# Kernel tuning notes

Hardware: AMD Instinct MI355X
Metric: run time of the kernel (lower is better)

Reference implementation:

```python
import jax, jax.numpy as jnp
import numpy as np

H, D, E, FOCAL, HID = 8, 32, 16, 4, 256  # heads, att_size, edge types, focal heads, hidden
SCALE = D ** -0.5
B, N = 16, 512


def setup_inputs() -> dict:
    key = jax.random.key(0)
    ks = jax.random.split(key, 16)
    f = lambda i, shape, s=1.0: jax.random.normal(ks[i], shape, jnp.float32) * s
    return {
        "q": f(0, (B, N, HID)),
        "k": f(1, (B, N, HID)),
        "v": f(2, (B, N, HID)),
        "query_edge_emb": f(3, (E, H * D), 0.1),
        "key_edge_emb": f(4, (E, H * D), 0.1),
        "edge_attr": jax.random.randint(ks[5], (B, N, N), 0, E),
        "mask": jax.random.randint(ks[6], (B, N), 0, 2).astype(bool),
        "focal_mask": jax.random.randint(ks[7], (B, N, N), 0, 2).astype(bool),
        "Wq": f(8, (H * D, HID), 0.05), "bq": jnp.zeros((H * D,), jnp.float32),
        "Wk": f(9, (H * D, HID), 0.05), "bk": jnp.zeros((H * D,), jnp.float32),
        "Wv": f(10, (H * D, HID), 0.05), "bv": jnp.zeros((H * D,), jnp.float32),
        "Wo": f(11, (HID, H * D), 0.05), "bo": jnp.zeros((HID,), jnp.float32),
    }


def reference(q, k, v, query_edge_emb, key_edge_emb, edge_attr, mask, focal_mask,
              Wq, bq, Wk, bk, Wv, bv, Wo, bo):
    b, n, _ = q.shape
    # projections -> [B, H, N, D]
    qh = (q @ Wq.T + bq).reshape(b, n, H, D).transpose(0, 2, 1, 3)
    kh = (k @ Wk.T + bk).reshape(b, n, H, D).transpose(0, 2, 1, 3)
    vh = (v @ Wv.T + bv).reshape(b, n, H, D).transpose(0, 2, 1, 3)

    # edge-type embeddings -> [H, E, D]
    qe_emb = query_edge_emb.reshape(E, H, D).transpose(1, 0, 2)
    ke_emb = key_edge_emb.reshape(E, H, D).transpose(1, 0, 2)

    # per-node score against each edge type: [B, H, N, E]
    qe = jnp.einsum('bhnd,hed->bhne', qh, qe_emb)
    ke = jnp.einsum('bhnd,hed->bhne', kh, ke_emb)

    # gather per edge type id: [B, H, N, N]
    idx = jnp.broadcast_to(edge_attr[:, None, :, :], (b, H, n, n))
    edge_bias = jnp.take_along_axis(qe, idx, axis=3) + jnp.take_along_axis(ke, idx, axis=3)

    attn = (jnp.einsum('bhid,bhjd->bhij', qh, kh) + edge_bias) * SCALE

    gh = H - FOCAL
    m_g = jnp.broadcast_to(mask[:, None, None, :], (b, gh, n, n))
    m_f = jnp.broadcast_to(focal_mask[:, None, :, :], (b, FOCAL, n, n))
    m = jnp.concatenate([m_g, m_f], axis=1)
    attn = jnp.where(m, attn, -jnp.inf)
    attn = jax.nn.softmax(attn, axis=3)

    out = jnp.einsum('bhij,bhjd->bhid', attn, vh)
    out = out.transpose(0, 2, 1, 3).reshape(b, n, H * D)
    return out @ Wo.T + bo
```

## Files before the change

### kernel.cpp

```cpp
#include <hip/hip_runtime.h>
#include <math.h>

namespace {

constexpr int B = 16, N = 512, H = 8, D = 32, E = 16, HID = 256;
constexpr float SCALE = 0.17677669529663687f;

typedef __attribute__((ext_vector_type(8))) short short8;
typedef __attribute__((ext_vector_type(4))) float float4v;

__device__ inline short f2bf(float x) {
  union { float f; unsigned u; } v; v.f = x;
  unsigned r = v.u + 0x7fffu + ((v.u >> 16) & 1u);
  return (short)(r >> 16);
}
__device__ inline float bf2f(unsigned short u) {
  union { unsigned u; float f; } v; v.u = ((unsigned)u) << 16; return v.f;
}

__global__ __launch_bounds__(256) void gemm_qkv(
    const float* __restrict__ Xq, const float* __restrict__ Xk, const float* __restrict__ Xv,
    const float* __restrict__ Wq, const float* __restrict__ Wk, const float* __restrict__ Wv,
    const float* __restrict__ bq, const float* __restrict__ bk, const float* __restrict__ bv,
    unsigned short* __restrict__ Ybase)
{
  __shared__ __align__(16) unsigned short As[64][72];
  __shared__ __align__(16) unsigned short Bs[64][72];
  const int z = blockIdx.z;
  const float* X = (z == 0) ? Xq : (z == 1) ? Xk : Xv;
  const float* W = (z == 0) ? Wq : (z == 1) ? Wk : Wv;
  const float* bias = (z == 0) ? bq : (z == 1) ? bk : bv;
  unsigned short* Yh = Ybase + (size_t)z * ((size_t)B * H * N * D);

  const int m0 = blockIdx.x * 64, n0 = blockIdx.y * 64;
  const int t = threadIdx.x, lane = t & 63, w = t >> 6;
  const int quad = lane >> 4, col = lane & 15;
  const int wm = (w & 1) * 32, wn = (w >> 1) * 32;
  const int srow = t >> 2, skk = (t & 3) * 16;
  float4v acc[2][2] = {{{0,0,0,0},{0,0,0,0}},{{0,0,0,0},{0,0,0,0}}};

  for (int kit = 0; kit < 4; ++kit) {
    const int k0 = kit * 64;
    {
      const float* xp = X + (size_t)(m0 + srow) * HID + k0 + skk;
      const float* wp = W + (size_t)(n0 + srow) * HID + k0 + skk;
      float4 x1 = *(const float4*)xp, x2 = *(const float4*)(xp + 4);
      float4 x3 = *(const float4*)(xp + 8), x4 = *(const float4*)(xp + 12);
      float4 w1 = *(const float4*)wp, w2 = *(const float4*)(wp + 4);
      float4 w3 = *(const float4*)(wp + 8), w4 = *(const float4*)(wp + 12);
      short8 xa, xb, wa, wb;
      xa[0]=f2bf(x1.x); xa[1]=f2bf(x1.y); xa[2]=f2bf(x1.z); xa[3]=f2bf(x1.w);
      xa[4]=f2bf(x2.x); xa[5]=f2bf(x2.y); xa[6]=f2bf(x2.z); xa[7]=f2bf(x2.w);
      xb[0]=f2bf(x3.x); xb[1]=f2bf(x3.y); xb[2]=f2bf(x3.z); xb[3]=f2bf(x3.w);
      xb[4]=f2bf(x4.x); xb[5]=f2bf(x4.y); xb[6]=f2bf(x4.z); xb[7]=f2bf(x4.w);
      wa[0]=f2bf(w1.x); wa[1]=f2bf(w1.y); wa[2]=f2bf(w1.z); wa[3]=f2bf(w1.w);
      wa[4]=f2bf(w2.x); wa[5]=f2bf(w2.y); wa[6]=f2bf(w2.z); wa[7]=f2bf(w2.w);
      wb[0]=f2bf(w3.x); wb[1]=f2bf(w3.y); wb[2]=f2bf(w3.z); wb[3]=f2bf(w3.w);
      wb[4]=f2bf(w4.x); wb[5]=f2bf(w4.y); wb[6]=f2bf(w4.z); wb[7]=f2bf(w4.w);
      *(short8*)&As[srow][skk] = xa; *(short8*)&As[srow][skk + 8] = xb;
      *(short8*)&Bs[srow][skk] = wa; *(short8*)&Bs[srow][skk + 8] = wb;
    }
    __syncthreads();
#pragma unroll
    for (int ks = 0; ks < 2; ++ks) {
      const int kk = ks * 32 + quad * 8;
      short8 a0 = *(const short8*)&As[wm + col][kk];
      short8 a1 = *(const short8*)&As[wm + 16 + col][kk];
      short8 b0 = *(const short8*)&Bs[wn + col][kk];
      short8 b1 = *(const short8*)&Bs[wn + 16 + col][kk];
      acc[0][0] = __builtin_amdgcn_mfma_f32_16x16x32_bf16(a0, b0, acc[0][0], 0, 0, 0);
      acc[0][1] = __builtin_amdgcn_mfma_f32_16x16x32_bf16(a0, b1, acc[0][1], 0, 0, 0);
      acc[1][0] = __builtin_amdgcn_mfma_f32_16x16x32_bf16(a1, b0, acc[1][0], 0, 0, 0);
      acc[1][1] = __builtin_amdgcn_mfma_f32_16x16x32_bf16(a1, b1, acc[1][1], 0, 0, 0);
    }
    __syncthreads();
  }
#pragma unroll
  for (int mt = 0; mt < 2; ++mt)
#pragma unroll
    for (int nt = 0; nt < 2; ++nt)
#pragma unroll
      for (int r = 0; r < 4; ++r) {
        const int m = m0 + wm + mt * 16 + quad * 4 + r;
        const int n = n0 + wn + nt * 16 + col;
        const float val = acc[mt][nt][r] + bias[n];
        const int b_ = m >> 9, ii = m & 511, h_ = n >> 5, d_ = n & 31;
        Yh[((size_t)(b_ * H + h_) * N + ii) * D + d_] = (unsigned short)f2bf(val);
      }
}

__global__ __launch_bounds__(256) void gemm_out(
    const unsigned short* __restrict__ X, const float* __restrict__ W,
    const float* __restrict__ bias, float* __restrict__ Yf)
{
  __shared__ __align__(16) unsigned short As[64][72];
  __shared__ __align__(16) unsigned short Bs[64][72];
  const int m0 = blockIdx.x * 64, n0 = blockIdx.y * 64;
  const int t = threadIdx.x, lane = t & 63, w = t >> 6;
  const int quad = lane >> 4, col = lane & 15;
  const int wm = (w & 1) * 32, wn = (w >> 1) * 32;
  const int srow = t >> 2, skk = (t & 3) * 16;
  float4v acc[2][2] = {{{0,0,0,0},{0,0,0,0}},{{0,0,0,0},{0,0,0,0}}};

  for (int kit = 0; kit < 4; ++kit) {
    const int k0 = kit * 64;
    {
      const unsigned short* xp = X + (size_t)(m0 + srow) * HID + k0 + skk;
      *(short8*)&As[srow][skk] = *(const short8*)xp;
      *(short8*)&As[srow][skk + 8] = *(const short8*)(xp + 8);
      const float* wp = W + (size_t)(n0 + srow) * HID + k0 + skk;
      float4 w1 = *(const float4*)wp, w2 = *(const float4*)(wp + 4);
      float4 w3 = *(const float4*)(wp + 8), w4 = *(const float4*)(wp + 12);
      short8 wa, wb;
      wa[0]=f2bf(w1.x); wa[1]=f2bf(w1.y); wa[2]=f2bf(w1.z); wa[3]=f2bf(w1.w);
      wa[4]=f2bf(w2.x); wa[5]=f2bf(w2.y); wa[6]=f2bf(w2.z); wa[7]=f2bf(w2.w);
      wb[0]=f2bf(w3.x); wb[1]=f2bf(w3.y); wb[2]=f2bf(w3.z); wb[3]=f2bf(w3.w);
      wb[4]=f2bf(w4.x); wb[5]=f2bf(w4.y); wb[6]=f2bf(w4.z); wb[7]=f2bf(w4.w);
      *(short8*)&Bs[srow][skk] = wa; *(short8*)&Bs[srow][skk + 8] = wb;
    }
    __syncthreads();
#pragma unroll
    for (int ks = 0; ks < 2; ++ks) {
      const int kk = ks * 32 + quad * 8;
      short8 a0 = *(const short8*)&As[wm + col][kk];
      short8 a1 = *(const short8*)&As[wm + 16 + col][kk];
      short8 b0 = *(const short8*)&Bs[wn + col][kk];
      short8 b1 = *(const short8*)&Bs[wn + 16 + col][kk];
      acc[0][0] = __builtin_amdgcn_mfma_f32_16x16x32_bf16(a0, b0, acc[0][0], 0, 0, 0);
      acc[0][1] = __builtin_amdgcn_mfma_f32_16x16x32_bf16(a0, b1, acc[0][1], 0, 0, 0);
      acc[1][0] = __builtin_amdgcn_mfma_f32_16x16x32_bf16(a1, b0, acc[1][0], 0, 0, 0);
      acc[1][1] = __builtin_amdgcn_mfma_f32_16x16x32_bf16(a1, b1, acc[1][1], 0, 0, 0);
    }
    __syncthreads();
  }
#pragma unroll
  for (int mt = 0; mt < 2; ++mt)
#pragma unroll
    for (int nt = 0; nt < 2; ++nt)
#pragma unroll
      for (int r = 0; r < 4; ++r) {
        const int m = m0 + wm + mt * 16 + quad * 4 + r;
        const int n = n0 + wn + nt * 16 + col;
        Yf[(size_t)m * HID + n] = acc[mt][nt][r] + bias[n];
      }
}

__global__ __launch_bounds__(256) void vtrans(
    const unsigned short* __restrict__ vh, unsigned short* __restrict__ vt)
{
  __shared__ unsigned short tile[32][522];
  const int t = threadIdx.x;
  const size_t base = (size_t)blockIdx.x * N * D;
  for (int idx = t; idx < N * D; idx += 256)
    tile[idx & 31][idx >> 5] = vh[base + idx];
  __syncthreads();
  for (int idx = t; idx < N * D; idx += 256)
    vt[base + idx] = tile[idx >> 9][idx & 511];
}

__global__ __launch_bounds__(256) void qke_kernel(
    const unsigned short* __restrict__ qh, const unsigned short* __restrict__ kh,
    const float* __restrict__ qemb, const float* __restrict__ kemb,
    float* __restrict__ qke)
{
  __shared__ float qs[512], ks[512];
  const int t = threadIdx.x;
  const int r0 = blockIdx.x * 16;
  const size_t base = (size_t)r0 * 32;
  for (int idx = t; idx < 512; idx += 256) {
    qs[idx] = bf2f(qh[base + idx]);
    ks[idx] = bf2f(kh[base + idx]);
  }
  __syncthreads();
  const int r = t >> 4, e = t & 15;
  const int h = ((r0 + r) >> 9) & 7;
  const float* qe = qemb + e * (H * D) + h * D;
  const float* ke = kemb + e * (H * D) + h * D;
  float a = 0.f;
#pragma unroll
  for (int d = 0; d < 32; ++d)
    a += qs[r * 32 + d] * qe[d] + ks[r * 32 + d] * ke[d];
  qke[(size_t)r0 * 16 + t] = a;
}

__global__ __launch_bounds__(256) void detect_bool(
    const unsigned int* __restrict__ buf, int* __restrict__ flag)
{
  __shared__ unsigned wr[4];
  const int t = threadIdx.x, w = t >> 6, lane = t & 63;
  unsigned v = 0;
  for (int idx = t; idx < 4096; idx += 256) v |= buf[idx];
  v |= __shfl_xor(v, 1);  v |= __shfl_xor(v, 2);  v |= __shfl_xor(v, 4);
  v |= __shfl_xor(v, 8);  v |= __shfl_xor(v, 16); v |= __shfl_xor(v, 32);
  if (lane == 0) wr[w] = v;
  __syncthreads();
  if (t == 0) flag[0] = ((wr[0] | wr[1] | wr[2] | wr[3]) > 1u) ? 1 : 0;
}

__global__ __launch_bounds__(256) void pack_kernel(
    const int* __restrict__ ea, const void* __restrict__ maskp,
    const void* __restrict__ fmaskp, const int* __restrict__ flag,
    unsigned char* __restrict__ packed)
{
  __shared__ unsigned char tl[16 * 520];
  const int it = blockIdx.x, b = blockIdx.y, t = threadIdx.x;
  const int i0 = it * 16;
  const int bf = *flag;
  const int* fm32 = (const int*)fmaskp;
  const unsigned char* fm8 = (const unsigned char*)fmaskp;
  const int* mk32 = (const int*)maskp;
  const unsigned char* mk8 = (const unsigned char*)maskp;

  for (int idx = t; idx < 16 * 512; idx += 256) {
    const int m = idx >> 9, j = idx & 511;
    const size_t goff = ((size_t)(b * N) + i0 + m) * N + j;
    const int e = ea[goff] & 15;
    const int fv = bf ? (int)fm8[goff] : fm32[goff];
    const int mv = bf ? (int)mk8[b * N + j] : mk32[b * N + j];
    tl[m * 520 + j] = (unsigned char)(e | (fv ? 16 : 0) | (mv ? 32 : 0));
  }
  __syncthreads();
#pragma unroll
  for (int rep = 0; rep < 2; ++rep) {
    const int j = t * 2 + rep;
    unsigned wd[4];
#pragma unroll
    for (int g = 0; g < 4; ++g) {
      const unsigned b0 = tl[(g * 4 + 0) * 520 + j];
      const unsigned b1 = tl[(g * 4 + 1) * 520 + j];
      const unsigned b2 = tl[(g * 4 + 2) * 520 + j];
      const unsigned b3 = tl[(g * 4 + 3) * 520 + j];
      wd[g] = b0 | (b1 << 8) | (b2 << 16) | (b3 << 24);
    }
    *(uint4*)(packed + ((size_t)(b * 32 + it) * 512 + j) * 16) =
        make_uint4(wd[0], wd[1], wd[2], wd[3]);
  }
}

__global__ __launch_bounds__(256, 3) void attn_mfma(
    const unsigned short* __restrict__ qh, const unsigned short* __restrict__ kh,
    const unsigned short* __restrict__ vt, const float* __restrict__ qke,
    const unsigned char* __restrict__ packed, unsigned short* __restrict__ ctx)
{
  __shared__ __align__(16) unsigned char tileT[512 * 16];
  __shared__ __align__(16) unsigned short P[4][16][136];
  __shared__ float qesS[2][16][17];
  __shared__ float ored[4][2][16][33];
  __shared__ float2 wlm[4][2][16];
  __shared__ float scl[4][32];
  __shared__ float linv[32];

  const int it = blockIdx.x, p = blockIdx.y, b = blockIdx.z;
  const int i0 = it * 16;
  const int t = threadIdx.x, w = t >> 6, lane = t & 63;
  const int quad = lane >> 4, col = lane & 15;

  {
    const unsigned char* pt = packed + ((size_t)(b * 32 + it) * 512) * 16;
    const int j0s = w * 128 + lane;
    *(uint4*)&tileT[(size_t)j0s * 16] = *(const uint4*)(pt + (size_t)j0s * 16);
    *(uint4*)&tileT[(size_t)(j0s + 64) * 16] =
        *(const uint4*)(pt + (size_t)(j0s + 64) * 16);
  }
#pragma unroll
  for (int rep = 0; rep < 2; ++rep) {
    const int vi = rep * 256 + t;
    const int h2 = vi >> 8, m = (vi >> 4) & 15, e = vi & 15;
    qesS[h2][m][e] =
        qke[((size_t)(b * H + p + h2 * 4) * N + i0 + m) * E + e] * SCALE;
  }
  __syncthreads();

#pragma unroll
  for (int h2 = 0; h2 < 2; ++h2) {
    const int bh = b * H + p + h2 * 4;
    const short8 qf = *(const short8*)(qh + ((size_t)bh * N + i0 + col) * D + quad * 8);

    float s[8][4];
#pragma unroll
    for (int c = 0; c < 8; ++c) {
      const int j0 = w * 128 + c * 16;
      const short8 kf = *(const short8*)(kh + ((size_t)bh * N + j0 + col) * D + quad * 8);
      float4v sc = {0, 0, 0, 0};
      sc = __builtin_amdgcn_mfma_f32_16x16x32_bf16(qf, kf, sc, 0, 0, 0);
      const unsigned pk = *(const unsigned*)&tileT[(size_t)(j0 + col) * 16 + quad * 4];
#pragma unroll
      for (int r = 0; r < 4; ++r) {
        const int m = quad * 4 + r;
        const unsigned by = pk >> (8 * r);
        const int e = by & 15;
        const int valid = h2 ? (by >> 4) & 1 : (by >> 5) & 1;
        const float sv = fmaf(sc[r], SCALE, qesS[h2][m][e]);
        s[c][r] = valid ? sv : -INFINITY;
      }
    }

    float mW[4];
#pragma unroll
    for (int r = 0; r < 4; ++r) {
      float m2 = s[0][r];
#pragma unroll
      for (int c = 1; c < 8; ++c) m2 = fmaxf(m2, s[c][r]);
      m2 = fmaxf(m2, __shfl_xor(m2, 1));
      m2 = fmaxf(m2, __shfl_xor(m2, 2));
      m2 = fmaxf(m2, __shfl_xor(m2, 4));
      m2 = fmaxf(m2, __shfl_xor(m2, 8));
      mW[r] = fmaxf(m2, -3.0e38f);
    }
#pragma unroll
    for (int r = 0; r < 4; ++r) {
      const int m = quad * 4 + r;
      float sm = 0.f;
#pragma unroll
      for (int c = 0; c < 8; ++c) {
        const float ex = __expf(s[c][r] - mW[r]);
        sm += ex;
        P[w][m][c * 16 + col] = (unsigned short)f2bf(ex);
      }
      sm += __shfl_xor(sm, 1);
      sm += __shfl_xor(sm, 2);
      sm += __shfl_xor(sm, 4);
      sm += __shfl_xor(sm, 8);
      if (col == 0) wlm[w][h2][m] = make_float2(mW[r], sm);
    }

    float4v o0 = {0, 0, 0, 0}, o1 = {0, 0, 0, 0};
#pragma unroll
    for (int c2 = 0; c2 < 4; ++c2) {
      const int kl = c2 * 32 + quad * 8;
      const short8 pf = *(const short8*)&P[w][col][kl];
      const int kg = w * 128 + kl;
      const short8 v0 = *(const short8*)(vt + ((size_t)bh * D + col) * N + kg);
      const short8 v1 = *(const short8*)(vt + ((size_t)bh * D + 16 + col) * N + kg);
      o0 = __builtin_amdgcn_mfma_f32_16x16x32_bf16(pf, v0, o0, 0, 0, 0);
      o1 = __builtin_amdgcn_mfma_f32_16x16x32_bf16(pf, v1, o1, 0, 0, 0);
    }
#pragma unroll
    for (int r = 0; r < 4; ++r) {
      ored[w][h2][quad * 4 + r][col] = o0[r];
      ored[w][h2][quad * 4 + r][col + 16] = o1[r];
    }
  }
  __syncthreads();

  if (t < 128) {
    const int u = t & 3, row = t >> 2, h2 = row >> 4, q = row & 15;
    const float2 s0 = wlm[0][h2][q], s1 = wlm[1][h2][q];
    const float2 s2 = wlm[2][h2][q], s3 = wlm[3][h2][q];
    const float mg = fmaxf(fmaxf(s0.x, s1.x), fmaxf(s2.x, s3.x));
    const float2 sw = (u == 0) ? s0 : (u == 1) ? s1 : (u == 2) ? s2 : s3;
    scl[u][row] = __expf(sw.x - mg);
    if (u == 0) {
      const float ls = s0.y * __expf(s0.x - mg) + s1.y * __expf(s1.x - mg) +
                       s2.y * __expf(s2.x - mg) + s3.y * __expf(s3.x - mg);
      linv[row] = 1.0f / ls;
    }
  }
  __syncthreads();

#pragma unroll
  for (int it2 = 0; it2 < 4; ++it2) {
    const int flat = it2 * 256 + t;
    const int h2 = flat >> 9, rem = flat & 511, q = rem >> 5, d = rem & 31;
    const int row = h2 * 16 + q;
    const float val = ored[0][h2][q][d] * scl[0][row] +
                      ored[1][h2][q][d] * scl[1][row] +
                      ored[2][h2][q][d] * scl[2][row] +
                      ored[3][h2][q][d] * scl[3][row];
    ctx[((size_t)(b * N) + i0 + q) * HID + (p + h2 * 4) * D + d] =
        (unsigned short)f2bf(val * linv[row]);
  }
}

}

extern "C" void kernel_launch(void* const* d_in, const int* in_sizes, int n_in,
                              void* d_out, int out_size, void* d_ws, size_t ws_size,
                              hipStream_t stream)
{
  const float* q    = (const float*)d_in[0];
  const float* k    = (const float*)d_in[1];
  const float* v    = (const float*)d_in[2];
  const float* qemb = (const float*)d_in[3];
  const float* kemb = (const float*)d_in[4];
  const int*   ea   = (const int*)d_in[5];
  const void*  mask = d_in[6];
  const void*  fmask= d_in[7];
  const float* Wq = (const float*)d_in[8];
  const float* bq = (const float*)d_in[9];
  const float* Wk = (const float*)d_in[10];
  const float* bk = (const float*)d_in[11];
  const float* Wv = (const float*)d_in[12];
  const float* bv = (const float*)d_in[13];
  const float* Wo = (const float*)d_in[14];
  const float* bo = (const float*)d_in[15];

  unsigned short* ws16 = (unsigned short*)d_ws;
  constexpr size_t HSZ = (size_t)B * H * N * D;
  unsigned short* qhb = ws16;
  unsigned short* khb = qhb + HSZ;
  unsigned short* vhb = khb + HSZ;
  unsigned short* vtb = vhb + HSZ;
  float* qkew = (float*)(ws16 + 4 * HSZ);
  unsigned short* ctx = (unsigned short*)(qkew + (size_t)B * H * N * E);
  unsigned char* packed = (unsigned char*)(ctx + (size_t)B * N * HID);
  int* flag = (int*)(packed + (size_t)B * N * N);

  gemm_qkv<<<dim3((B * N) / 64, HID / 64, 3), 256, 0, stream>>>(
      q, k, v, Wq, Wk, Wv, bq, bk, bv, qhb);
  detect_bool<<<1, 256, 0, stream>>>((const unsigned int*)fmask, flag);
  pack_kernel<<<dim3(N / 16, B), 256, 0, stream>>>(ea, mask, fmask, flag, packed);
  vtrans<<<B * H, 256, 0, stream>>>(vhb, vtb);
  qke_kernel<<<(B * H * N) / 16, 256, 0, stream>>>(qhb, khb, qemb, kemb, qkew);
  attn_mfma<<<dim3(N / 16, H / 2, B), 256, 0, stream>>>(qhb, khb, vtb, qkew,
                                                        packed, ctx);
  gemm_out<<<dim3((B * N) / 64, HID / 64), 256, 0, stream>>>(ctx, Wo, bo, (float*)d_out);
}
```

Baseline: 226.5 us.

## Pre-convert inputs to bf16, fuse V transpose into QKV GEMM, vectorize pack

Adds a conversion kernel that turns q/k/v and all weights into bf16 once and also does the bool-mask detection, which removes the detect_bool launch. The QKV and output GEMMs now load bf16 directly instead of converting fp32 in their inner loops. The V projection writes its transposed layout directly, which drops the separate vtrans kernel. pack_kernel reads edge and mask data with vector loads. The cost is an extra full read/write pass over the inputs and uncoalesced 2-byte strided stores for the transposed V.

```diff
diff --git a/kernel.cpp b/kernel.cpp
--- a/kernel.cpp
+++ b/kernel.cpp
@@ -5,6 +5,8 @@
 
 constexpr int B = 16, N = 512, H = 8, D = 32, E = 16, HID = 256;
 constexpr float SCALE = 0.17677669529663687f;
+constexpr size_t HSZ = (size_t)B * H * N * D;
+constexpr size_t WSZ = (size_t)HID * HID;
 
 typedef __attribute__((ext_vector_type(8))) short short8;
 typedef __attribute__((ext_vector_type(4))) float float4v;
@@ -18,19 +20,64 @@
   union { unsigned u; float f; } v; v.u = ((unsigned)u) << 16; return v.f;
 }
 
+__global__ __launch_bounds__(256) void convert_kernel(
+    const float* __restrict__ q, const float* __restrict__ k, const float* __restrict__ v,
+    const float* __restrict__ Wq, const float* __restrict__ Wk,
+    const float* __restrict__ Wv, const float* __restrict__ Wo,
+    unsigned short* __restrict__ qx, unsigned short* __restrict__ kx,
+    unsigned short* __restrict__ vx, unsigned short* __restrict__ wq,
+    unsigned short* __restrict__ wk, unsigned short* __restrict__ wv,
+    unsigned short* __restrict__ wo,
+    const unsigned* __restrict__ fmask_u32, int* __restrict__ flag)
+{
+  if (blockIdx.x == gridDim.x - 1) {
+    __shared__ unsigned wr[4];
+    const int t = threadIdx.x, w = t >> 6, lane = t & 63;
+    unsigned o = 0;
+    for (int idx = t; idx < 4096; idx += 256) o |= fmask_u32[idx];
+    o |= __shfl_xor(o, 1);  o |= __shfl_xor(o, 2);  o |= __shfl_xor(o, 4);
+    o |= __shfl_xor(o, 8);  o |= __shfl_xor(o, 16); o |= __shfl_xor(o, 32);
+    if (lane == 0) wr[w] = o;
+    __syncthreads();
+    if (t == 0) flag[0] = ((wr[0] | wr[1] | wr[2] | wr[3]) > 1u) ? 1 : 0;
+    return;
+  }
+  constexpr size_t H4 = HSZ / 4;
+  constexpr size_t W4 = WSZ / 4;
+  const size_t idx = (size_t)blockIdx.x * 256 + threadIdx.x;
+  const float* src; unsigned short* dst; size_t off;
+  if (idx < H4)            { src = q; dst = qx; off = idx; }
+  else if (idx < 2 * H4)   { src = k; dst = kx; off = idx - H4; }
+  else if (idx < 3 * H4)   { src = v; dst = vx; off = idx - 2 * H4; }
+  else {
+    const size_t r = idx - 3 * H4;
+    const int wsel = (int)(r / W4); off = r % W4;
+    src = (wsel == 0) ? Wq : (wsel == 1) ? Wk : (wsel == 2) ? Wv : Wo;
+    dst = (wsel == 0) ? wq : (wsel == 1) ? wk : (wsel == 2) ? wv : wo;
+  }
+  const float4 f = ((const float4*)src)[off];
+  ushort4 o;
+  o.x = (unsigned short)f2bf(f.x); o.y = (unsigned short)f2bf(f.y);
+  o.z = (unsigned short)f2bf(f.z); o.w = (unsigned short)f2bf(f.w);
+  ((ushort4*)dst)[off] = o;
+}
+
 __global__ __launch_bounds__(256) void gemm_qkv(
-    const float* __restrict__ Xq, const float* __restrict__ Xk, const float* __restrict__ Xv,
-    const float* __restrict__ Wq, const float* __restrict__ Wk, const float* __restrict__ Wv,
-    const float* __restrict__ bq, const float* __restrict__ bk, const float* __restrict__ bv,
-    unsigned short* __restrict__ Ybase)
+    const unsigned short* __restrict__ Xq, const unsigned short* __restrict__ Xk,
+    const unsigned short* __restrict__ Xv,
+    const unsigned short* __restrict__ Wq, const unsigned short* __restrict__ Wk,
+    const unsigned short* __restrict__ Wv,
+    const float* __restrict__ bq, const float* __restrict__ bk,
+    const float* __restrict__ bv,
+    unsigned short* __restrict__ qh, unsigned short* __restrict__ kh,
+    unsigned short* __restrict__ vt)
 {
   __shared__ __align__(16) unsigned short As[64][72];
   __shared__ __align__(16) unsigned short Bs[64][72];
   const int z = blockIdx.z;
-  const float* X = (z == 0) ? Xq : (z == 1) ? Xk : Xv;
-  const float* W = (z == 0) ? Wq : (z == 1) ? Wk : Wv;
+  const unsigned short* X = (z == 0) ? Xq : (z == 1) ? Xk : Xv;
+  const unsigned short* W = (z == 0) ? Wq : (z == 1) ? Wk : Wv;
   const float* bias = (z == 0) ? bq : (z == 1) ? bk : bv;
-  unsigned short* Yh = Ybase + (size_t)z * ((size_t)B * H * N * D);
 
   const int m0 = blockIdx.x * 64, n0 = blockIdx.y * 64;
   const int t = threadIdx.x, lane = t & 63, w = t >> 6;
@@ -42,23 +89,12 @@
   for (int kit = 0; kit < 4; ++kit) {
     const int k0 = kit * 64;
     {
-      const float* xp = X + (size_t)(m0 + srow) * HID + k0 + skk;
-      const float* wp = W + (size_t)(n0 + srow) * HID + k0 + skk;
-      float4 x1 = *(const float4*)xp, x2 = *(const float4*)(xp + 4);
-      float4 x3 = *(const float4*)(xp + 8), x4 = *(const float4*)(xp + 12);
-      float4 w1 = *(const float4*)wp, w2 = *(const float4*)(wp + 4);
-      float4 w3 = *(const float4*)(wp + 8), w4 = *(const float4*)(wp + 12);
-      short8 xa, xb, wa, wb;
-      xa[0]=f2bf(x1.x); xa[1]=f2bf(x1.y); xa[2]=f2bf(x1.z); xa[3]=f2bf(x1.w);
-      xa[4]=f2bf(x2.x); xa[5]=f2bf(x2.y); xa[6]=f2bf(x2.z); xa[7]=f2bf(x2.w);
-      xb[0]=f2bf(x3.x); xb[1]=f2bf(x3.y); xb[2]=f2bf(x3.z); xb[3]=f2bf(x3.w);
-      xb[4]=f2bf(x4.x); xb[5]=f2bf(x4.y); xb[6]=f2bf(x4.z); xb[7]=f2bf(x4.w);
-      wa[0]=f2bf(w1.x); wa[1]=f2bf(w1.y); wa[2]=f2bf(w1.z); wa[3]=f2bf(w1.w);
-      wa[4]=f2bf(w2.x); wa[5]=f2bf(w2.y); wa[6]=f2bf(w2.z); wa[7]=f2bf(w2.w);
-      wb[0]=f2bf(w3.x); wb[1]=f2bf(w3.y); wb[2]=f2bf(w3.z); wb[3]=f2bf(w3.w);
-      wb[4]=f2bf(w4.x); wb[5]=f2bf(w4.y); wb[6]=f2bf(w4.z); wb[7]=f2bf(w4.w);
-      *(short8*)&As[srow][skk] = xa; *(short8*)&As[srow][skk + 8] = xb;
-      *(short8*)&Bs[srow][skk] = wa; *(short8*)&Bs[srow][skk + 8] = wb;
+      const unsigned short* xp = X + (size_t)(m0 + srow) * HID + k0 + skk;
+      const unsigned short* wp = W + (size_t)(n0 + srow) * HID + k0 + skk;
+      *(short8*)&As[srow][skk] = *(const short8*)xp;
+      *(short8*)&As[srow][skk + 8] = *(const short8*)(xp + 8);
+      *(short8*)&Bs[srow][skk] = *(const short8*)wp;
+      *(short8*)&Bs[srow][skk + 8] = *(const short8*)(wp + 8);
     }
     __syncthreads();
 #pragma unroll
@@ -85,12 +121,17 @@
         const int n = n0 + wn + nt * 16 + col;
         const float val = acc[mt][nt][r] + bias[n];
         const int b_ = m >> 9, ii = m & 511, h_ = n >> 5, d_ = n & 31;
-        Yh[((size_t)(b_ * H + h_) * N + ii) * D + d_] = (unsigned short)f2bf(val);
+        if (z == 2) {
+          vt[((size_t)(b_ * H + h_) * D + d_) * N + ii] = (unsigned short)f2bf(val);
+        } else {
+          unsigned short* Yh = (z == 0) ? qh : kh;
+          Yh[((size_t)(b_ * H + h_) * N + ii) * D + d_] = (unsigned short)f2bf(val);
+        }
       }
 }
 
 __global__ __launch_bounds__(256) void gemm_out(
-    const unsigned short* __restrict__ X, const float* __restrict__ W,
+    const unsigned short* __restrict__ X, const unsigned short* __restrict__ W,
     const float* __restrict__ bias, float* __restrict__ Yf)
 {
   __shared__ __align__(16) unsigned short As[64][72];
@@ -106,17 +147,11 @@
     const int k0 = kit * 64;
     {
       const unsigned short* xp = X + (size_t)(m0 + srow) * HID + k0 + skk;
+      const unsigned short* wp = W + (size_t)(n0 + srow) * HID + k0 + skk;
       *(short8*)&As[srow][skk] = *(const short8*)xp;
       *(short8*)&As[srow][skk + 8] = *(const short8*)(xp + 8);
-      const float* wp = W + (size_t)(n0 + srow) * HID + k0 + skk;
-      float4 w1 = *(const float4*)wp, w2 = *(const float4*)(wp + 4);
-      float4 w3 = *(const float4*)(wp + 8), w4 = *(const float4*)(wp + 12);
-      short8 wa, wb;
-      wa[0]=f2bf(w1.x); wa[1]=f2bf(w1.y); wa[2]=f2bf(w1.z); wa[3]=f2bf(w1.w);
-      wa[4]=f2bf(w2.x); wa[5]=f2bf(w2.y); wa[6]=f2bf(w2.z); wa[7]=f2bf(w2.w);
-      wb[0]=f2bf(w3.x); wb[1]=f2bf(w3.y); wb[2]=f2bf(w3.z); wb[3]=f2bf(w3.w);
-      wb[4]=f2bf(w4.x); wb[5]=f2bf(w4.y); wb[6]=f2bf(w4.z); wb[7]=f2bf(w4.w);
-      *(short8*)&Bs[srow][skk] = wa; *(short8*)&Bs[srow][skk + 8] = wb;
+      *(short8*)&Bs[srow][skk] = *(const short8*)wp;
+      *(short8*)&Bs[srow][skk + 8] = *(const short8*)(wp + 8);
     }
     __syncthreads();
 #pragma unroll
@@ -145,19 +180,6 @@
       }
 }
 
-__global__ __launch_bounds__(256) void vtrans(
-    const unsigned short* __restrict__ vh, unsigned short* __restrict__ vt)
-{
-  __shared__ unsigned short tile[32][522];
-  const int t = threadIdx.x;
-  const size_t base = (size_t)blockIdx.x * N * D;
-  for (int idx = t; idx < N * D; idx += 256)
-    tile[idx & 31][idx >> 5] = vh[base + idx];
-  __syncthreads();
-  for (int idx = t; idx < N * D; idx += 256)
-    vt[base + idx] = tile[idx >> 9][idx & 511];
-}
-
 __global__ __launch_bounds__(256) void qke_kernel(
     const unsigned short* __restrict__ qh, const unsigned short* __restrict__ kh,
     const float* __restrict__ qemb, const float* __restrict__ kemb,
@@ -181,20 +203,6 @@
   for (int d = 0; d < 32; ++d)
     a += qs[r * 32 + d] * qe[d] + ks[r * 32 + d] * ke[d];
   qke[(size_t)r0 * 16 + t] = a;
-}
-
-__global__ __launch_bounds__(256) void detect_bool(
-    const unsigned int* __restrict__ buf, int* __restrict__ flag)
-{
-  __shared__ unsigned wr[4];
-  const int t = threadIdx.x, w = t >> 6, lane = t & 63;
-  unsigned v = 0;
-  for (int idx = t; idx < 4096; idx += 256) v |= buf[idx];
-  v |= __shfl_xor(v, 1);  v |= __shfl_xor(v, 2);  v |= __shfl_xor(v, 4);
-  v |= __shfl_xor(v, 8);  v |= __shfl_xor(v, 16); v |= __shfl_xor(v, 32);
-  if (lane == 0) wr[w] = v;
-  __syncthreads();
-  if (t == 0) flag[0] = ((wr[0] | wr[1] | wr[2] | wr[3]) > 1u) ? 1 : 0;
 }
 
 __global__ __launch_bounds__(256) void pack_kernel(
@@ -211,13 +219,27 @@
   const int* mk32 = (const int*)maskp;
   const unsigned char* mk8 = (const unsigned char*)maskp;
 
-  for (int idx = t; idx < 16 * 512; idx += 256) {
-    const int m = idx >> 9, j = idx & 511;
-    const size_t goff = ((size_t)(b * N) + i0 + m) * N + j;
-    const int e = ea[goff] & 15;
-    const int fv = bf ? (int)fm8[goff] : fm32[goff];
-    const int mv = bf ? (int)mk8[b * N + j] : mk32[b * N + j];
-    tl[m * 520 + j] = (unsigned char)(e | (fv ? 16 : 0) | (mv ? 32 : 0));
+  for (int idx4 = t; idx4 < 2048; idx4 += 256) {
+    const int m = idx4 >> 7, j4 = (idx4 & 127) * 4;
+    const size_t rowoff = ((size_t)(b * N) + i0 + m) * N;
+    const int4 e4 = *(const int4*)(ea + rowoff + j4);
+    int fv0, fv1, fv2, fv3, mv0, mv1, mv2, mv3;
+    if (bf) {
+      const unsigned fw = *(const unsigned*)(fm8 + rowoff + j4);
+      fv0 = fw & 0xff; fv1 = (fw >> 8) & 0xff; fv2 = (fw >> 16) & 0xff; fv3 = fw >> 24;
+      const unsigned mw = *(const unsigned*)(mk8 + b * N + j4);
+      mv0 = mw & 0xff; mv1 = (mw >> 8) & 0xff; mv2 = (mw >> 16) & 0xff; mv3 = mw >> 24;
+    } else {
+      const int4 fw = *(const int4*)(fm32 + rowoff + j4);
+      fv0 = fw.x; fv1 = fw.y; fv2 = fw.z; fv3 = fw.w;
+      const int4 mw = *(const int4*)(mk32 + b * N + j4);
+      mv0 = mw.x; mv1 = mw.y; mv2 = mw.z; mv3 = mw.w;
+    }
+    const unsigned b0 = (e4.x & 15) | (fv0 ? 16u : 0u) | (mv0 ? 32u : 0u);
+    const unsigned b1 = (e4.y & 15) | (fv1 ? 16u : 0u) | (mv1 ? 32u : 0u);
+    const unsigned b2 = (e4.z & 15) | (fv2 ? 16u : 0u) | (mv2 ? 32u : 0u);
+    const unsigned b3 = (e4.w & 15) | (fv3 ? 16u : 0u) | (mv3 ? 32u : 0u);
+    *(unsigned*)&tl[m * 520 + j4] = b0 | (b1 << 8) | (b2 << 16) | (b3 << 24);
   }
   __syncthreads();
 #pragma unroll
@@ -226,11 +248,11 @@
     unsigned wd[4];
 #pragma unroll
     for (int g = 0; g < 4; ++g) {
-      const unsigned b0 = tl[(g * 4 + 0) * 520 + j];
-      const unsigned b1 = tl[(g * 4 + 1) * 520 + j];
-      const unsigned b2 = tl[(g * 4 + 2) * 520 + j];
-      const unsigned b3 = tl[(g * 4 + 3) * 520 + j];
-      wd[g] = b0 | (b1 << 8) | (b2 << 16) | (b3 << 24);
+      const unsigned c0 = tl[(g * 4 + 0) * 520 + j];
+      const unsigned c1 = tl[(g * 4 + 1) * 520 + j];
+      const unsigned c2 = tl[(g * 4 + 2) * 520 + j];
+      const unsigned c3 = tl[(g * 4 + 3) * 520 + j];
+      wd[g] = c0 | (c1 << 8) | (c2 << 16) | (c3 << 24);
     }
     *(uint4*)(packed + ((size_t)(b * 32 + it) * 512 + j) * 16) =
         make_uint4(wd[0], wd[1], wd[2], wd[3]);
@@ -396,23 +418,29 @@
   const float* bo = (const float*)d_in[15];
 
   unsigned short* ws16 = (unsigned short*)d_ws;
-  constexpr size_t HSZ = (size_t)B * H * N * D;
   unsigned short* qhb = ws16;
   unsigned short* khb = qhb + HSZ;
-  unsigned short* vhb = khb + HSZ;
-  unsigned short* vtb = vhb + HSZ;
-  float* qkew = (float*)(ws16 + 4 * HSZ);
+  unsigned short* vtb = khb + HSZ;
+  float* qkew = (float*)(vtb + HSZ);
   unsigned short* ctx = (unsigned short*)(qkew + (size_t)B * H * N * E);
   unsigned char* packed = (unsigned char*)(ctx + (size_t)B * N * HID);
-  int* flag = (int*)(packed + (size_t)B * N * N);
-
+  unsigned short* qxb = (unsigned short*)(packed + (size_t)B * N * N);
+  unsigned short* kxb = qxb + HSZ;
+  unsigned short* vxb = kxb + HSZ;
+  unsigned short* wqb = vxb + HSZ;
+  unsigned short* wkb = wqb + WSZ;
+  unsigned short* wvb = wkb + WSZ;
+  unsigned short* wob = wvb + WSZ;
+  int* flag = (int*)(wob + WSZ);
+
+  convert_kernel<<<6401, 256, 0, stream>>>(q, k, v, Wq, Wk, Wv, Wo,
+                                           qxb, kxb, vxb, wqb, wkb, wvb, wob,
+                                           (const unsigned*)fmask, flag);
+  pack_kernel<<<dim3(N / 16, B), 256, 0, stream>>>(ea, mask, fmask, flag, packed);
   gemm_qkv<<<dim3((B * N) / 64, HID / 64, 3), 256, 0, stream>>>(
-      q, k, v, Wq, Wk, Wv, bq, bk, bv, qhb);
-  detect_bool<<<1, 256, 0, stream>>>((const unsigned int*)fmask, flag);
-  pack_kernel<<<dim3(N / 16, B), 256, 0, stream>>>(ea, mask, fmask, flag, packed);
-  vtrans<<<B * H, 256, 0, stream>>>(vhb, vtb);
+      qxb, kxb, vxb, wqb, wkb, wvb, bq, bk, bv, qhb, khb, vtb);
   qke_kernel<<<(B * H * N) / 16, 256, 0, stream>>>(qhb, khb, qemb, kemb, qkew);
   attn_mfma<<<dim3(N / 16, H / 2, B), 256, 0, stream>>>(qhb, khb, vtb, qkew,
                                                         packed, ctx);
-  gemm_out<<<dim3((B * N) / 64, HID / 64), 256, 0, stream>>>(ctx, Wo, bo, (float*)d_out);
-}
+  gemm_out<<<dim3((B * N) / 64, HID / 64), 256, 0, stream>>>(ctx, wob, bo, (float*)d_out);
+}
```

After: 212.3 us. -6.3%, faster.
